# Kernel optimization log

Hardware: AMD Instinct MI355X
Metric: run time of the kernel (lower is better)

Reference implementation:

```python
import jax, jax.numpy as jnp
import numpy as np

INPUT_SIZE = 40960
HIDDEN = 256
MAX_FEATS = 32
BATCH = 8192


def setup_inputs() -> dict:
    key = jax.random.key(0)
    ks = jax.random.split(key, 10)
    wf = jax.random.randint(ks[0], (BATCH, MAX_FEATS), 0, INPUT_SIZE, dtype=jnp.int64 if jax.config.jax_enable_x64 else jnp.int32)
    bf = jax.random.randint(ks[1], (BATCH, MAX_FEATS), 0, INPUT_SIZE, dtype=wf.dtype)
    pad_w = jax.random.uniform(ks[2], (BATCH, MAX_FEATS)) < 0.25
    pad_b = jax.random.uniform(ks[3], (BATCH, MAX_FEATS)) < 0.25
    wf = jnp.where(pad_w, -1, wf)
    bf = jnp.where(pad_b, -1, bf)
    stm = jax.random.bernoulli(ks[4], 0.5, (BATCH,)).astype(jnp.float32)
    # Parameters (torch Linear convention: weight [out, in]).
    bound = 1.0 / np.sqrt(INPUT_SIZE)
    ft_W = jax.random.uniform(ks[5], (HIDDEN, INPUT_SIZE), jnp.float32, -bound, bound)
    ft_b = jnp.zeros((HIDDEN,), jnp.float32)
    w1 = jax.random.normal(ks[6], (32, HIDDEN * 2), jnp.float32) * np.sqrt(2.0 / (HIDDEN * 2))
    b1 = jnp.zeros((32,), jnp.float32)
    w2 = jax.random.normal(ks[7], (32, 32), jnp.float32) * np.sqrt(2.0 / 32)
    b2 = jnp.zeros((32,), jnp.float32)
    wo = jax.random.uniform(ks[8], (1, 32), jnp.float32, -0.1, 0.1)
    bo = jnp.zeros((1,), jnp.float32)
    return {"white_features": wf, "black_features": bf, "stm": stm,
            "ft_W": ft_W, "ft_b": ft_b, "w1": w1, "b1": b1,
            "w2": w2, "b2": b2, "wo": wo, "bo": bo}


def _accumulate(idx, ft_Wt, ft_b):
    # idx: [B, F] with -1 padding; ft_Wt: [INPUT_SIZE, HIDDEN]
    valid = (idx >= 0)
    idxc = jnp.clip(idx, 0, INPUT_SIZE - 1)
    g = ft_Wt[idxc] * valid[..., None].astype(ft_Wt.dtype)  # [B, F, H]
    return g.sum(axis=1) + ft_b  # [B, H]


def reference(white_features, black_features, stm, ft_W, ft_b, w1, b1, w2, b2, wo, bo):
    ft_Wt = ft_W.T  # [INPUT_SIZE, HIDDEN]
    wh = _accumulate(white_features, ft_Wt, ft_b)
    bh = _accumulate(black_features, ft_Wt, ft_b)
    # clamp(relu(x), 0, 127) == clip(x, 0, 127)
    wh = jnp.clip(wh, 0.0, 127.0)
    bh = jnp.clip(bh, 0.0, 127.0)
    s = stm[:, None]
    us = s * wh + (1.0 - s) * bh
    them = s * bh + (1.0 - s) * wh
    x = jnp.concatenate([us, them], axis=1)  # [B, 2H]
    x = jax.nn.relu(x @ w1.T + b1)
    x = jax.nn.relu(x @ w2.T + b2)
    x = x @ wo.T + bo  # [B, 1]
    return jax.nn.sigmoid(x.squeeze(-1))
```

## Files before the change

### kernel.cpp

```cpp
#include <hip/hip_runtime.h>
#include <math.h>

#define BATCH   8192
#define HIDDEN  256
#define MAXF    32
#define ISZ     40960
#define BPB     4
#define TF      128

#define QSCALE  7.842927e-5f
#define INVQ    1.2750335e+4f

__global__ __launch_bounds__(256) void transpose_q(const float* __restrict__ src,
                                                   signed char* __restrict__ dstq,
                                                   const float* __restrict__ w1,
                                                   const float* __restrict__ w2,
                                                   float* __restrict__ w1t,
                                                   float* __restrict__ w2t) {
    if (blockIdx.x == ISZ / TF) {
        for (int i = threadIdx.x; i < 32 * 512; i += 256) {
            int j = i >> 9, k = i & 511;
            w1t[k * 32 + j] = w1[i];
        }
        for (int i = threadIdx.x; i < 32 * 32; i += 256) {
            int j = i >> 5, k = i & 31;
            w2t[k * 32 + j] = w2[i];
        }
        return;
    }

    __shared__ short tile[TF][260];
    const int t    = threadIdx.x;
    const int wave = t >> 6;
    const int lane = t & 63;
    const int F0   = blockIdx.x * TF;
    const int hw   = lane >> 5;
    const int l32  = lane & 31;

#pragma unroll 4
    for (int i = 0; i < 32; ++i) {
        const int h = i * 8 + wave * 2 + hw;
        const float4 v = *(const float4*)&src[(size_t)h * ISZ + F0 + 4 * l32];
        int q0 = __float2int_rn(v.x * INVQ); q0 = max(-127, min(127, q0));
        int q1 = __float2int_rn(v.y * INVQ); q1 = max(-127, min(127, q1));
        int q2 = __float2int_rn(v.z * INVQ); q2 = max(-127, min(127, q2));
        int q3 = __float2int_rn(v.w * INVQ); q3 = max(-127, min(127, q3));
        tile[4 * l32 + 0][h] = (short)q0;
        tile[4 * l32 + 1][h] = (short)q1;
        tile[4 * l32 + 2][h] = (short)q2;
        tile[4 * l32 + 3][h] = (short)q3;
    }
    __syncthreads();

    unsigned int* dq = (unsigned int*)dstq;
    for (int f = wave; f < TF; f += 4) {
        const short4 q = *(const short4*)&tile[f][4 * lane];
        unsigned int p = (q.x & 0xFF) | ((q.y & 0xFF) << 8) |
                         ((q.z & 0xFF) << 16) | ((unsigned int)(q.w & 0xFF) << 24);
        dq[(size_t)(F0 + f) * 64 + lane] = p;
    }
}

__global__ __launch_bounds__(256) void nnue_fused_q(
    const int* __restrict__ wf, const int* __restrict__ bfeat,
    const float* __restrict__ stm,
    const signed char* __restrict__ ftQ,
    const float* __restrict__ ftb,
    const float* __restrict__ w1, const float* __restrict__ b1,
    const float* __restrict__ w2, const float* __restrict__ b2,
    const float* __restrict__ wo, const float* __restrict__ bo,
    float* __restrict__ out) {

    __shared__ float sX[BPB][512];
    __shared__ float sP[2][BPB][32];
    __shared__ float sY2[BPB][32];

    const int  t       = threadIdx.x;
    const int  wave    = t >> 6;
    const int  lane    = t & 63;
    const int  l32     = lane & 31;
    const bool isWhite = lane < 32;
    const int  b       = blockIdx.x * BPB + wave;

    int myidx = isWhite ? wf[b * MAXF + l32] : bfeat[b * MAXF + l32];

    int acc[8];
#pragma unroll
    for (int j = 0; j < 8; ++j) acc[j] = 0;

    const uint2* ftQ2 = (const uint2*)ftQ;

#pragma unroll 16
    for (int f = 0; f < MAXF; ++f) {
        const int iw  = __builtin_amdgcn_readlane(myidx, f);
        const int ib  = __builtin_amdgcn_readlane(myidx, f + 32);
        const int row = isWhite ? iw : ib;
        const int rc  = row < 0 ? 0 : row;
        uint2 d = ftQ2[(size_t)rc * 32 + l32];
        if (row < 0) { d.x = 0u; d.y = 0u; }
#pragma unroll
        for (int k = 0; k < 4; ++k) acc[k]     += (int)(signed char)(d.x >> (8 * k));
#pragma unroll
        for (int k = 0; k < 4; ++k) acc[4 + k] += (int)(signed char)(d.y >> (8 * k));
    }

    const float4 tb0 = ((const float4*)ftb)[2 * l32];
    const float4 tb1 = ((const float4*)ftb)[2 * l32 + 1];
    float h[8];
    h[0] = (float)acc[0] * QSCALE + tb0.x;
    h[1] = (float)acc[1] * QSCALE + tb0.y;
    h[2] = (float)acc[2] * QSCALE + tb0.z;
    h[3] = (float)acc[3] * QSCALE + tb0.w;
    h[4] = (float)acc[4] * QSCALE + tb1.x;
    h[5] = (float)acc[5] * QSCALE + tb1.y;
    h[6] = (float)acc[6] * QSCALE + tb1.z;
    h[7] = (float)acc[7] * QSCALE + tb1.w;
#pragma unroll
    for (int j = 0; j < 8; ++j) h[j] = fminf(fmaxf(h[j], 0.f), 127.f);

    const float s   = stm[b];
    const int   off = (isWhite == (s > 0.5f)) ? 0 : 256;
    *(float4*)&sX[wave][off + 8 * l32]     = make_float4(h[0], h[1], h[2], h[3]);
    *(float4*)&sX[wave][off + 8 * l32 + 4] = make_float4(h[4], h[5], h[6], h[7]);
    __syncthreads();

    {
        const int j  = t & 31;
        const int q  = (t >> 5) & (BPB - 1);
        const int kh = t >> 7;
        const float* x = sX[q];
        float y = kh ? 0.0f : b1[j];
        const int k0 = kh * 256;
#pragma unroll 8
        for (int kk = 0; kk < 256; ++kk) {
            const int k = k0 + kk;
            y = fmaf(x[k], w1[k * 32 + j], y);
        }
        sP[kh][q][j] = y;
    }
    __syncthreads();

    if (t < BPB * 32) {
        const int q = t >> 5, j = t & 31;
        float y = b2[j];
#pragma unroll
        for (int k = 0; k < 32; ++k) {
            float x1 = fmaxf(sP[0][q][k] + sP[1][q][k], 0.0f);
            y = fmaf(x1, w2[k * 32 + j], y);
        }
        sY2[q][j] = fmaxf(y, 0.0f);
    }
    __syncthreads();

    if (t < BPB) {
        float y = bo[0];
#pragma unroll
        for (int k = 0; k < 32; ++k) y = fmaf(sY2[t][k], wo[k], y);
        out[blockIdx.x * BPB + t] = 1.0f / (1.0f + expf(-y));
    }
}

__global__ __launch_bounds__(256) void nnue_fused_fb(
    const int* __restrict__ wf, const int* __restrict__ bfeat,
    const float* __restrict__ stm,
    const float* __restrict__ ftW, const float* __restrict__ ftb,
    const float* __restrict__ w1, const float* __restrict__ b1,
    const float* __restrict__ w2, const float* __restrict__ b2,
    const float* __restrict__ wo, const float* __restrict__ bo,
    float* __restrict__ out) {

    __shared__ float sX[BPB][512];
    __shared__ float sP[2][BPB][32];
    __shared__ float sY2[BPB][32];

    const int t = threadIdx.x, wave = t >> 6, lane = t & 63;
    const int b = blockIdx.x * BPB + wave;
    int myidx = (lane < 32) ? wf[b * MAXF + lane] : bfeat[b * MAXF + (lane - 32)];
    const float4* ftb4 = (const float4*)ftb;
    float4 accw = ftb4[lane];
    float4 accb = accw;

    for (int f = 0; f < MAXF; ++f) {
        int iw = __builtin_amdgcn_readlane(myidx, f);
        int ib = __builtin_amdgcn_readlane(myidx, f + 32);
        float mw = (iw >= 0) ? 1.0f : 0.0f;
        float mb = (ib >= 0) ? 1.0f : 0.0f;
        int iwc = iw < 0 ? 0 : iw;
        int ibc = ib < 0 ? 0 : ib;
#pragma unroll
        for (int c = 0; c < 4; ++c) {
            float gw = ftW[(size_t)(4 * lane + c) * ISZ + iwc];
            float gb = ftW[(size_t)(4 * lane + c) * ISZ + ibc];
            float* aw = (c == 0) ? &accw.x : (c == 1) ? &accw.y : (c == 2) ? &accw.z : &accw.w;
            float* ab = (c == 0) ? &accb.x : (c == 1) ? &accb.y : (c == 2) ? &accb.z : &accb.w;
            *aw = fmaf(gw, mw, *aw);
            *ab = fmaf(gb, mb, *ab);
        }
    }
#pragma unroll
    for (int c = 0; c < 4; ++c) {
        float* aw = (c == 0) ? &accw.x : (c == 1) ? &accw.y : (c == 2) ? &accw.z : &accw.w;
        float* ab = (c == 0) ? &accb.x : (c == 1) ? &accb.y : (c == 2) ? &accb.z : &accb.w;
        *aw = fminf(fmaxf(*aw, 0.f), 127.f);
        *ab = fminf(fmaxf(*ab, 0.f), 127.f);
    }
    float s = stm[b];
    float4 us, th;
    if (s > 0.5f) { us = accw; th = accb; } else { us = accb; th = accw; }
    ((float4*)sX[wave])[lane] = us;
    ((float4*)sX[wave])[64 + lane] = th;
    __syncthreads();
    {
        const int j = t & 31, q = (t >> 5) & (BPB - 1), kh = t >> 7;
        const float* x = sX[q];
        float y = kh ? 0.0f : b1[j];
        const int k0 = kh * 256;
        for (int kk = 0; kk < 256; ++kk) {
            const int k = k0 + kk;
            y = fmaf(x[k], w1[j * 512 + k], y);
        }
        sP[kh][q][j] = y;
    }
    __syncthreads();
    if (t < BPB * 32) {
        const int q = t >> 5, j = t & 31;
        float y = b2[j];
        for (int k = 0; k < 32; ++k) {
            float x1 = fmaxf(sP[0][q][k] + sP[1][q][k], 0.0f);
            y = fmaf(x1, w2[j * 32 + k], y);
        }
        sY2[q][j] = fmaxf(y, 0.0f);
    }
    __syncthreads();
    if (t < BPB) {
        float y = bo[0];
        for (int k = 0; k < 32; ++k) y = fmaf(sY2[t][k], wo[k], y);
        out[blockIdx.x * BPB + t] = 1.0f / (1.0f + expf(-y));
    }
}

extern "C" void kernel_launch(void* const* d_in, const int* in_sizes, int n_in,
                              void* d_out, int out_size, void* d_ws, size_t ws_size,
                              hipStream_t stream) {
    const int*   wf  = (const int*)d_in[0];
    const int*   bfe = (const int*)d_in[1];
    const float* stm = (const float*)d_in[2];
    const float* ftW = (const float*)d_in[3];
    const float* ftb = (const float*)d_in[4];
    const float* w1  = (const float*)d_in[5];
    const float* b1  = (const float*)d_in[6];
    const float* w2  = (const float*)d_in[7];
    const float* b2  = (const float*)d_in[8];
    const float* wo  = (const float*)d_in[9];
    const float* bo  = (const float*)d_in[10];
    float* out = (float*)d_out;

    const size_t ftQ_bytes = (size_t)ISZ * HIDDEN;
    const size_t w1t_bytes = 512 * 32 * 4;
    const size_t w2t_bytes = 32 * 32 * 4;
    const size_t need      = ftQ_bytes + w1t_bytes + w2t_bytes;

    if (ws_size >= need) {
        signed char* ftQ = (signed char*)d_ws;
        float* w1t = (float*)((char*)d_ws + ftQ_bytes);
        float* w2t = w1t + 512 * 32;
        transpose_q<<<ISZ / TF + 1, 256, 0, stream>>>(ftW, ftQ, w1, w2, w1t, w2t);
        nnue_fused_q<<<BATCH / BPB, 256, 0, stream>>>(
            wf, bfe, stm, ftQ, ftb, w1t, b1, w2t, b2, wo, bo, out);
    } else {
        nnue_fused_fb<<<BATCH / BPB, 256, 0, stream>>>(
            wf, bfe, stm, ftW, ftb, w1, b1, w2, b2, wo, bo, out);
    }
}
```

Before: 146.7 us.

## Use offset-binary int8 with packed SWAR accumulation and 8 items per block

The int8 feature table is stored offset by 128 as unsigned bytes. The gather loop can then accumulate two 16-bit lanes per 32-bit add (SWAR) from 16-byte loads, with 16 lanes covering a row and 4 rows processed per wave, instead of sign-extending each byte. Each block now handles 8 batch items with indices staged in shared memory. The first dense layer reads w1 in a k-chunked float4 layout, so each thread does a full 512-long dot product and the split-K partial reduction is gone. Padding entries are replaced by 0x80 bytes, and a constant offset is subtracted from the bias to undo the 128 shift.

```diff
diff --git a/kernel.cpp b/kernel.cpp
--- a/kernel.cpp
+++ b/kernel.cpp
@@ -5,22 +5,22 @@
 #define HIDDEN  256
 #define MAXF    32
 #define ISZ     40960
-#define BPB     4
 #define TF      128
 
 #define QSCALE  7.842927e-5f
 #define INVQ    1.2750335e+4f
+#define QOFF    (4096.0f * QSCALE)
 
 __global__ __launch_bounds__(256) void transpose_q(const float* __restrict__ src,
-                                                   signed char* __restrict__ dstq,
+                                                   unsigned char* __restrict__ dstq,
                                                    const float* __restrict__ w1,
                                                    const float* __restrict__ w2,
-                                                   float* __restrict__ w1t,
+                                                   float* __restrict__ w1c,
                                                    float* __restrict__ w2t) {
     if (blockIdx.x == ISZ / TF) {
         for (int i = threadIdx.x; i < 32 * 512; i += 256) {
             int j = i >> 9, k = i & 511;
-            w1t[k * 32 + j] = w1[i];
+            w1c[(k >> 2) * 128 + j * 4 + (k & 3)] = w1[i];
         }
         for (int i = threadIdx.x; i < 32 * 32; i += 256) {
             int j = i >> 5, k = i & 31;
@@ -41,10 +41,10 @@
     for (int i = 0; i < 32; ++i) {
         const int h = i * 8 + wave * 2 + hw;
         const float4 v = *(const float4*)&src[(size_t)h * ISZ + F0 + 4 * l32];
-        int q0 = __float2int_rn(v.x * INVQ); q0 = max(-127, min(127, q0));
-        int q1 = __float2int_rn(v.y * INVQ); q1 = max(-127, min(127, q1));
-        int q2 = __float2int_rn(v.z * INVQ); q2 = max(-127, min(127, q2));
-        int q3 = __float2int_rn(v.w * INVQ); q3 = max(-127, min(127, q3));
+        int q0 = __float2int_rn(v.x * INVQ); q0 = max(-127, min(127, q0)) + 128;
+        int q1 = __float2int_rn(v.y * INVQ); q1 = max(-127, min(127, q1)) + 128;
+        int q2 = __float2int_rn(v.z * INVQ); q2 = max(-127, min(127, q2)) + 128;
+        int q3 = __float2int_rn(v.w * INVQ); q3 = max(-127, min(127, q3)) + 128;
         tile[4 * l32 + 0][h] = (short)q0;
         tile[4 * l32 + 1][h] = (short)q1;
         tile[4 * l32 + 2][h] = (short)q2;
@@ -64,99 +64,102 @@
 __global__ __launch_bounds__(256) void nnue_fused_q(
     const int* __restrict__ wf, const int* __restrict__ bfeat,
     const float* __restrict__ stm,
-    const signed char* __restrict__ ftQ,
+    const unsigned char* __restrict__ ftQ,
     const float* __restrict__ ftb,
-    const float* __restrict__ w1, const float* __restrict__ b1,
-    const float* __restrict__ w2, const float* __restrict__ b2,
-    const float* __restrict__ wo, const float* __restrict__ bo,
+    const float* __restrict__ w1c, const float* __restrict__ b1,
+    const float* __restrict__ w2,  const float* __restrict__ b2,
+    const float* __restrict__ wo,  const float* __restrict__ bo,
     float* __restrict__ out) {
 
-    __shared__ float sX[BPB][512];
-    __shared__ float sP[2][BPB][32];
-    __shared__ float sY2[BPB][32];
-
-    const int  t       = threadIdx.x;
-    const int  wave    = t >> 6;
-    const int  lane    = t & 63;
-    const int  l32     = lane & 31;
-    const bool isWhite = lane < 32;
-    const int  b       = blockIdx.x * BPB + wave;
-
-    int myidx = isWhite ? wf[b * MAXF + l32] : bfeat[b * MAXF + l32];
-
-    int acc[8];
-#pragma unroll
-    for (int j = 0; j < 8; ++j) acc[j] = 0;
-
-    const uint2* ftQ2 = (const uint2*)ftQ;
-
-#pragma unroll 16
+    __shared__ int   sIdx[4][32][4];
+    __shared__ float sX[8][512];
+    __shared__ float sY1[8][32];
+    __shared__ float sY2[8][32];
+
+    const int t    = threadIdx.x;
+    const int wave = t >> 6;
+    const int lane = t & 63;
+    const int g    = lane >> 4;
+    const int c16  = lane & 15;
+    const int ib0  = blockIdx.x * 8;
+
+    {
+        const int item = t >> 5, f = t & 31;
+        sIdx[item >> 1][f][(item & 1) * 2 + 0] = wf   [(ib0 + item) * MAXF + f];
+        sIdx[item >> 1][f][(item & 1) * 2 + 1] = bfeat[(ib0 + item) * MAXF + f];
+    }
+    __syncthreads();
+
+    unsigned acc[8];
+#pragma unroll
+    for (int k = 0; k < 8; ++k) acc[k] = 0u;
+
+    const uint4* T = (const uint4*)ftQ;
+
+#pragma unroll 8
     for (int f = 0; f < MAXF; ++f) {
-        const int iw  = __builtin_amdgcn_readlane(myidx, f);
-        const int ib  = __builtin_amdgcn_readlane(myidx, f + 32);
-        const int row = isWhite ? iw : ib;
-        const int rc  = row < 0 ? 0 : row;
-        uint2 d = ftQ2[(size_t)rc * 32 + l32];
-        if (row < 0) { d.x = 0u; d.y = 0u; }
-#pragma unroll
-        for (int k = 0; k < 4; ++k) acc[k]     += (int)(signed char)(d.x >> (8 * k));
-#pragma unroll
-        for (int k = 0; k < 4; ++k) acc[4 + k] += (int)(signed char)(d.y >> (8 * k));
-    }
-
-    const float4 tb0 = ((const float4*)ftb)[2 * l32];
-    const float4 tb1 = ((const float4*)ftb)[2 * l32 + 1];
-    float h[8];
-    h[0] = (float)acc[0] * QSCALE + tb0.x;
-    h[1] = (float)acc[1] * QSCALE + tb0.y;
-    h[2] = (float)acc[2] * QSCALE + tb0.z;
-    h[3] = (float)acc[3] * QSCALE + tb0.w;
-    h[4] = (float)acc[4] * QSCALE + tb1.x;
-    h[5] = (float)acc[5] * QSCALE + tb1.y;
-    h[6] = (float)acc[6] * QSCALE + tb1.z;
-    h[7] = (float)acc[7] * QSCALE + tb1.w;
-#pragma unroll
-    for (int j = 0; j < 8; ++j) h[j] = fminf(fmaxf(h[j], 0.f), 127.f);
-
-    const float s   = stm[b];
-    const int   off = (isWhite == (s > 0.5f)) ? 0 : 256;
-    *(float4*)&sX[wave][off + 8 * l32]     = make_float4(h[0], h[1], h[2], h[3]);
-    *(float4*)&sX[wave][off + 8 * l32 + 4] = make_float4(h[4], h[5], h[6], h[7]);
-    __syncthreads();
-
-    {
-        const int j  = t & 31;
-        const int q  = (t >> 5) & (BPB - 1);
-        const int kh = t >> 7;
-        const float* x = sX[q];
-        float y = kh ? 0.0f : b1[j];
-        const int k0 = kh * 256;
-#pragma unroll 8
-        for (int kk = 0; kk < 256; ++kk) {
-            const int k = k0 + kk;
-            y = fmaf(x[k], w1[k * 32 + j], y);
-        }
-        sP[kh][q][j] = y;
-    }
-    __syncthreads();
-
-    if (t < BPB * 32) {
-        const int q = t >> 5, j = t & 31;
+        const int idx = sIdx[wave][f][g];
+        const int rc  = idx < 0 ? 0 : idx;
+        uint4 d = T[rc * 16 + c16];
+        if (idx < 0) { d.x = 0x80808080u; d.y = 0x80808080u;
+                       d.z = 0x80808080u; d.w = 0x80808080u; }
+        acc[0] += d.x & 0x00FF00FFu;  acc[1] += (d.x >> 8) & 0x00FF00FFu;
+        acc[2] += d.y & 0x00FF00FFu;  acc[3] += (d.y >> 8) & 0x00FF00FFu;
+        acc[4] += d.z & 0x00FF00FFu;  acc[5] += (d.z >> 8) & 0x00FF00FFu;
+        acc[6] += d.w & 0x00FF00FFu;  acc[7] += (d.w >> 8) & 0x00FF00FFu;
+    }
+
+    const float4* ftb4 = (const float4*)ftb;
+    float h[16];
+#pragma unroll
+    for (int m = 0; m < 4; ++m) {
+        const float4 tb = ftb4[c16 * 4 + m];
+        h[4*m+0] = (float)(acc[2*m]     & 0xFFFFu) * QSCALE + (tb.x - QOFF);
+        h[4*m+1] = (float)(acc[2*m + 1] & 0xFFFFu) * QSCALE + (tb.y - QOFF);
+        h[4*m+2] = (float)(acc[2*m]    >> 16)      * QSCALE + (tb.z - QOFF);
+        h[4*m+3] = (float)(acc[2*m + 1] >> 16)     * QSCALE + (tb.w - QOFF);
+    }
+#pragma unroll
+    for (int u = 0; u < 16; ++u) h[u] = fminf(fmaxf(h[u], 0.f), 127.f);
+
+    const int   li  = wave * 2 + (g >> 1);
+    const float s   = stm[ib0 + li];
+    const int   off = (((g & 1) == 0) == (s > 0.5f)) ? 0 : 256;
+    float* xrow = &sX[li][off + 16 * c16];
+#pragma unroll
+    for (int m = 0; m < 4; ++m)
+        *(float4*)&xrow[4 * m] = make_float4(h[4*m], h[4*m+1], h[4*m+2], h[4*m+3]);
+    __syncthreads();
+
+    {
+        const int j = t & 31, q = t >> 5;
+        const float4* w1c4 = (const float4*)w1c;
+        float y = b1[j];
+#pragma unroll 4
+        for (int ks = 0; ks < 128; ++ks) {
+            const float4 x4 = *(const float4*)&sX[q][4 * ks];
+            const float4 wv = w1c4[ks * 32 + j];
+            y = fmaf(x4.x, wv.x, y); y = fmaf(x4.y, wv.y, y);
+            y = fmaf(x4.z, wv.z, y); y = fmaf(x4.w, wv.w, y);
+        }
+        sY1[q][j] = fmaxf(y, 0.0f);
+    }
+    __syncthreads();
+
+    {
+        const int j = t & 31, q = t >> 5;
         float y = b2[j];
 #pragma unroll
-        for (int k = 0; k < 32; ++k) {
-            float x1 = fmaxf(sP[0][q][k] + sP[1][q][k], 0.0f);
-            y = fmaf(x1, w2[k * 32 + j], y);
-        }
+        for (int k = 0; k < 32; ++k) y = fmaf(sY1[q][k], w2[k * 32 + j], y);
         sY2[q][j] = fmaxf(y, 0.0f);
     }
     __syncthreads();
 
-    if (t < BPB) {
+    if (t < 8) {
         float y = bo[0];
 #pragma unroll
         for (int k = 0; k < 32; ++k) y = fmaf(sY2[t][k], wo[k], y);
-        out[blockIdx.x * BPB + t] = 1.0f / (1.0f + expf(-y));
+        out[ib0 + t] = 1.0f / (1.0f + expf(-y));
     }
 }
 
@@ -169,12 +172,12 @@
     const float* __restrict__ wo, const float* __restrict__ bo,
     float* __restrict__ out) {
 
-    __shared__ float sX[BPB][512];
-    __shared__ float sP[2][BPB][32];
-    __shared__ float sY2[BPB][32];
+    __shared__ float sX[4][512];
+    __shared__ float sP[2][4][32];
+    __shared__ float sY2[4][32];
 
     const int t = threadIdx.x, wave = t >> 6, lane = t & 63;
-    const int b = blockIdx.x * BPB + wave;
+    const int b = blockIdx.x * 4 + wave;
     int myidx = (lane < 32) ? wf[b * MAXF + lane] : bfeat[b * MAXF + (lane - 32)];
     const float4* ftb4 = (const float4*)ftb;
     float4 accw = ftb4[lane];
@@ -211,7 +214,7 @@
     ((float4*)sX[wave])[64 + lane] = th;
     __syncthreads();
     {
-        const int j = t & 31, q = (t >> 5) & (BPB - 1), kh = t >> 7;
+        const int j = t & 31, q = (t >> 5) & 3, kh = t >> 7;
         const float* x = sX[q];
         float y = kh ? 0.0f : b1[j];
         const int k0 = kh * 256;
@@ -222,7 +225,7 @@
         sP[kh][q][j] = y;
     }
     __syncthreads();
-    if (t < BPB * 32) {
+    if (t < 128) {
         const int q = t >> 5, j = t & 31;
         float y = b2[j];
         for (int k = 0; k < 32; ++k) {
@@ -232,10 +235,10 @@
         sY2[q][j] = fmaxf(y, 0.0f);
     }
     __syncthreads();
-    if (t < BPB) {
+    if (t < 4) {
         float y = bo[0];
         for (int k = 0; k < 32; ++k) y = fmaf(sY2[t][k], wo[k], y);
-        out[blockIdx.x * BPB + t] = 1.0f / (1.0f + expf(-y));
+        out[blockIdx.x * 4 + t] = 1.0f / (1.0f + expf(-y));
     }
 }
 
@@ -256,19 +259,19 @@
     float* out = (float*)d_out;
 
     const size_t ftQ_bytes = (size_t)ISZ * HIDDEN;
-    const size_t w1t_bytes = 512 * 32 * 4;
+    const size_t w1c_bytes = 512 * 32 * 4;
     const size_t w2t_bytes = 32 * 32 * 4;
-    const size_t need      = ftQ_bytes + w1t_bytes + w2t_bytes;
+    const size_t need      = ftQ_bytes + w1c_bytes + w2t_bytes;
 
     if (ws_size >= need) {
-        signed char* ftQ = (signed char*)d_ws;
-        float* w1t = (float*)((char*)d_ws + ftQ_bytes);
-        float* w2t = w1t + 512 * 32;
-        transpose_q<<<ISZ / TF + 1, 256, 0, stream>>>(ftW, ftQ, w1, w2, w1t, w2t);
-        nnue_fused_q<<<BATCH / BPB, 256, 0, stream>>>(
-            wf, bfe, stm, ftQ, ftb, w1t, b1, w2t, b2, wo, bo, out);
+        unsigned char* ftQ = (unsigned char*)d_ws;
+        float* w1c = (float*)((char*)d_ws + ftQ_bytes);
+        float* w2t = w1c + 512 * 32;
+        transpose_q<<<ISZ / TF + 1, 256, 0, stream>>>(ftW, ftQ, w1, w2, w1c, w2t);
+        nnue_fused_q<<<BATCH / 8, 256, 0, stream>>>(
+            wf, bfe, stm, ftQ, ftb, w1c, b1, w2t, b2, wo, bo, out);
     } else {
-        nnue_fused_fb<<<BATCH / BPB, 256, 0, stream>>>(
+        nnue_fused_fb<<<BATCH / 4, 256, 0, stream>>>(
             wf, bfe, stm, ftW, ftb, w1, b1, w2, b2, wo, bo, out);
     }
 }
```

Measured after the change: 133.1 us. 1.1x faster.
